# Performance work log

Hardware: AMD Instinct MI355X
Metric: run time of the kernel (lower is better)

## Reference

```python
import jax, jax.numpy as jnp
import numpy as np
import math

SR = 16000
WIN = 320
HOP = 160
NFFT = 512
NMEL = 64
PREEMPH = 0.97
LOG_GUARD = 2.0 ** (-24)
PAD_TO = 16
EPS = 1e-5  # CONSTANT added to std


def _slaney_mel_fbanks(sr=SR, n_fft=NFFT, n_mels=NMEL, fmin=0.0, fmax=8000.0):
    """Replicates torchaudio.functional.melscale_fbanks(norm='slaney', mel_scale='slaney').
    Returns [n_mels, n_freqs] (already transposed like the torch buffer `fb`)."""
    n_freqs = n_fft // 2 + 1
    all_freqs = np.linspace(0.0, sr / 2.0, n_freqs)
    f_sp = 200.0 / 3.0
    min_log_hz = 1000.0
    min_log_mel = min_log_hz / f_sp
    logstep = math.log(6.4) / 27.0

    def hz2mel(f):
        f = np.asarray(f, dtype=np.float64)
        return np.where(f >= min_log_hz,
                        min_log_mel + np.log(np.maximum(f, 1e-10) / min_log_hz) / logstep,
                        f / f_sp)

    def mel2hz(m):
        m = np.asarray(m, dtype=np.float64)
        return np.where(m >= min_log_mel,
                        min_log_hz * np.exp(logstep * (m - min_log_mel)),
                        f_sp * m)

    m_pts = np.linspace(hz2mel(fmin), hz2mel(fmax), n_mels + 2)
    f_pts = mel2hz(m_pts)                       # [n_mels+2]
    f_diff = f_pts[1:] - f_pts[:-1]             # [n_mels+1]
    slopes = f_pts[None, :] - all_freqs[:, None]  # [n_freqs, n_mels+2]
    down = -slopes[:, :-2] / f_diff[:-1]
    up = slopes[:, 2:] / f_diff[1:]
    fb = np.maximum(0.0, np.minimum(down, up))  # [n_freqs, n_mels]
    enorm = 2.0 / (f_pts[2:] - f_pts[:-2])      # slaney area normalization
    fb = fb * enorm[None, :]
    return fb.T.astype(np.float32)              # [n_mels, n_freqs]


def _hann_window_padded(win_length=WIN, n_fft=NFFT):
    # the window symmetrically to n_fft.
    w = np.hanning(win_length).astype(np.float32)
    left = (n_fft - win_length) // 2
    out = np.zeros(n_fft, dtype=np.float32)
    out[left:left + win_length] = w
    return out


def setup_inputs() -> dict:
    key = jax.random.key(0)
    kx, kl = jax.random.split(key)
    B, L = 32, 256000
    x = jax.random.normal(kx, (B, L), dtype=jnp.float32)
    # ragged valid lengths in [L/2, L] (plenty of frames per feature)
    seq_len = jax.random.randint(kl, (B,), L // 2, L + 1, dtype=jnp.int32)
    window = jnp.asarray(_hann_window_padded())       # [NFFT]
    fb = jnp.asarray(_slaney_mel_fbanks())            # [NMEL, NFFT//2+1]
    return {"x": x, "seq_len": seq_len, "window": window, "fb": fb}


def _forward(x, seq_len, window, fb):
    B, L = x.shape
    # get_seq_len: pad_amount = 2*(n_fft//2); floor((L + pad - n_fft)/hop) + 1
    feat_len = (seq_len + NFFT - NFFT) // HOP + 1     # = seq_len // HOP + 1
    # pre-emphasis
    x = jnp.concatenate([x[:, :1], x[:, 1:] - PREEMPH * x[:, :-1]], axis=1)
    # STFT, center=True reflect padding (eval mode: no dither)
    pad = NFFT // 2
    xp = jnp.pad(x, ((0, 0), (pad, pad)), mode='reflect')
    T = L // HOP + 1                                  # 1601 frames
    idx = jnp.arange(T)[:, None] * HOP + jnp.arange(NFFT)[None, :]
    frames = xp[:, idx] * window                      # [B, T, NFFT]
    spec = jnp.fft.rfft(frames, axis=-1)              # [B, T, F]
    # magnitude then mag_power=2 -> power spectrum (guard=0 since use_grads=False)
    pow_spec = spec.real ** 2 + spec.imag ** 2        # [B, T, F]
    mel = jnp.einsum('mf,btf->bmt', fb, pow_spec)     # [B, NMEL, T]
    logmel = jnp.log(mel + LOG_GUARD)
    # per_feature masked normalization (torch.std is unbiased -> /(n-1)), std += 1e-5
    mask = (jnp.arange(T)[None, :] < feat_len[:, None])          # [B, T]
    m = mask[:, None, :].astype(logmel.dtype)                    # [B, 1, T]
    n = feat_len.astype(logmel.dtype)[:, None, None]
    mean = jnp.sum(logmel * m, axis=2, keepdims=True) / n
    var = jnp.sum(((logmel - mean) * m) ** 2, axis=2, keepdims=True) / (n - 1.0)
    std = jnp.sqrt(var) + EPS
    out = (logmel - mean) / std
    # fill padding frames with pad_value=0
    out = jnp.where(m > 0, out, 0.0)
    # pad time dim to a multiple of pad_to=16 with pad_value
    pad_amt = (-T) % PAD_TO
    out = jnp.pad(out, ((0, 0), (0, 0), (0, pad_amt)), constant_values=0.0)
    return out, feat_len


def reference(x, seq_len, window, fb):
    return _forward(x, seq_len, window, fb)
```

## Files before the change

### kernel.cpp

```cpp
#include <hip/hip_runtime.h>
#include <math.h>

#define L_IN 256000
#define T_FR 1601
#define T_PAD 1616
#define NMEL_K 64
#define F_BINS 257
#define HOP_K 160
#define PRE_E 0.97f
#define LOG_GUARD_K 5.9604644775390625e-08f
#define FPB 16
#define CONC 4
#define GROUPS 101
#define SPAN 2912

__device__ __forceinline__ float2 cmulf(float2 a, float2 b) {
  return make_float2(a.x * b.x - a.y * b.y, a.x * b.y + a.y * b.x);
}

__global__ void prep_kernel(const float* __restrict__ fb, float* __restrict__ fbc,
                            int* __restrict__ loAlG) {
  const int m = blockIdx.x;
  const int t = threadIdx.x;
  int first = 512, last = -1;
  for (int c = 0; c < 5; ++c) {
    int f = t + 64 * c;
    if (f < F_BINS) {
      float v = fb[m * F_BINS + f];
      if (v > 0.0f) { first = min(first, f); last = max(last, f); }
    }
  }
  for (int off = 32; off > 0; off >>= 1) {
    first = min(first, __shfl_xor(first, off));
    last = max(last, __shfl_xor(last, off));
  }
  int lo = (first <= last) ? first : 0;
  int lastv = (first <= last) ? last : 0;
  int la = lo & ~3;
  if (t == 0) loAlG[m] = la;
  if (t < 32) {
    int f = la + t;
    float v = (f >= lo && f <= lastv && f < F_BINS) ? fb[m * F_BINS + f] : 0.0f;
    fbc[m * 32 + t] = v;
  }
}

__global__ void __launch_bounds__(256) frame_fft_mel_kernel(
    const float* __restrict__ x, const float* __restrict__ window,
    const float* __restrict__ fbc, const int* __restrict__ loAlG,
    float* __restrict__ out) {
  __shared__ __align__(16) float xs[SPAN];
  __shared__ __align__(16) float pw[CONC][288];
  __shared__ float outm[NMEL_K][FPB + 1];

  const int tid = threadIdx.x;
  const int w = tid >> 6;
  const int lane = tid & 63;
  const int b = blockIdx.x / GROUPS;
  const int g = blockIdx.x - b * GROUPS;
  const int t0 = g * FPB;
  const float* xb = x + (size_t)b * L_IN;
  const int base = t0 * HOP_K - 256;

  for (int n = tid; n < SPAN; n += 256) {
    int i = base + n;
    i = (i < 0) ? -i : i;
    i = (i >= L_IN) ? (2 * L_IN - 2 - i) : i;
    xs[n] = (i == 0) ? xb[0] : fmaf(-PRE_E, xb[i - 1], xb[i]);
  }

  const int sig = __builtin_bitreverse32(lane) >> 26;
  float wr[4], wi[4];
#pragma unroll
  for (int q = 0; q < 4; ++q) {
    float2 wv = *(const float2*)(window + 2 * (lane + 64 * q));
    wr[q] = wv.x; wi[q] = wv.y;
  }
  float2 tw1, tw2, tw3;
  {
    float a = -0.024543692606170259f * (float)lane;
    __sincosf(a, &tw1.y, &tw1.x);
    tw2 = cmulf(tw1, tw1);
    tw3 = cmulf(tw2, tw1);
  }
  float stc[6], sts[6];
#pragma unroll
  for (int i = 0; i < 6; ++i) {
    int H = 32 >> i;
    int p = lane & (H - 1);
    float a = -3.14159265358979323846f * (float)p / (float)H;
    __sincosf(a, &sts[i], &stc[i]);
  }
  float cu[4], su[4];
  {
    float a = -0.049087385212340519f * (float)sig;
    float cb, sb;
    __sincosf(a, &sb, &cb);
    const float C[4] = {1.0f, 0.99992470183914454f, 0.99969881869620425f, 0.99932238458834954f};
    const float S[4] = {0.0f, 0.01227153828571993f, 0.02454122852291229f, 0.03680722294135883f};
#pragma unroll
    for (int r = 0; r < 4; ++r) {
      cu[r] = cb * C[r] + sb * S[r];
      su[r] = sb * C[r] - cb * S[r];
    }
  }
  const int idx0 = __builtin_bitreverse32((64 - sig) & 63) >> 26;
  const int la = loAlG[lane];
  const float4* fr4 = (const float4*)fbc + lane * 8;

  __syncthreads();

  for (int c = 0; c < FPB / CONC; ++c) {
    const int j = c * CONC + w;
    const int off = j * HOP_K;

    float Br[4], Bi[4];
    {
      float zr[4], zi[4];
#pragma unroll
      for (int q = 0; q < 4; ++q) {
        float2 v = *(const float2*)(xs + off + 2 * (lane + 64 * q));
        zr[q] = v.x * wr[q];
        zi[q] = v.y * wi[q];
      }
      float e0r = zr[0] + zr[2], e0i = zi[0] + zi[2];
      float e1r = zr[1] + zr[3], e1i = zi[1] + zi[3];
      float d0r = zr[0] - zr[2], d0i = zi[0] - zi[2];
      float d1r = zr[1] - zr[3], d1i = zi[1] - zi[3];
      Br[0] = e0r + e1r; Bi[0] = e0i + e1i;
      float A2r = e0r - e1r, A2i = e0i - e1i;
      float A1r = d0r + d1i, A1i = d0i - d1r;
      float A3r = d0r - d1i, A3i = d0i + d1r;
      Br[1] = A1r * tw1.x - A1i * tw1.y; Bi[1] = A1r * tw1.y + A1i * tw1.x;
      Br[2] = A2r * tw2.x - A2i * tw2.y; Bi[2] = A2r * tw2.y + A2i * tw2.x;
      Br[3] = A3r * tw3.x - A3i * tw3.y; Bi[3] = A3r * tw3.y + A3i * tw3.x;
    }

#pragma unroll
    for (int i = 0; i < 6; ++i) {
      const int H = 32 >> i;
      const bool hi = (lane & H) != 0;
      const float cc = stc[i], ss = sts[i];
#pragma unroll
      for (int r = 0; r < 4; ++r) {
        float tr = __shfl_xor(Br[r], H);
        float ti = __shfl_xor(Bi[r], H);
        float sr = Br[r] + tr, si = Bi[r] + ti;
        float dr = tr - Br[r], di = ti - Bi[r];
        float pr = dr * cc - di * ss, pi = dr * ss + di * cc;
        Br[r] = hi ? pr : sr;
        Bi[r] = hi ? pi : si;
      }
    }

    {
      float q3r = __shfl_xor(Br[3], 63), q3i = __shfl_xor(Bi[3], 63);
      float q2r = __shfl_xor(Br[2], 63), q2i = __shfl_xor(Bi[2], 63);
      float q1r = __shfl_xor(Br[1], 63), q1i = __shfl_xor(Bi[1], 63);
      float q0r = __shfl(Br[0], idx0), q0i = __shfl(Bi[0], idx0);
      float qr[4] = {q0r, q3r, q2r, q1r};
      float qi_[4] = {q0i, q3i, q2i, q1i};
      float pv[4];
#pragma unroll
      for (int r = 0; r < 4; ++r) {
        float Er = 0.5f * (Br[r] + qr[r]);
        float Ei = 0.5f * (Bi[r] - qi_[r]);
        float Or = 0.5f * (Bi[r] + qi_[r]);
        float Oi = 0.5f * (qr[r] - Br[r]);
        float Xr = Er + cu[r] * Or - su[r] * Oi;
        float Xi = Ei + cu[r] * Oi + su[r] * Or;
        pv[r] = Xr * Xr + Xi * Xi;
      }
      ((float4*)pw[w])[sig] = make_float4(pv[0], pv[1], pv[2], pv[3]);
      if (lane == 0) { float d = Br[0] - Bi[0]; pw[w][256] = d * d; }
      else if (lane < 32) pw[w][256 + lane] = 0.0f;
    }
    __builtin_amdgcn_wave_barrier();

    {
      const float4* pq = (const float4*)pw[w] + (la >> 2);
      float acc = 0.0f;
#pragma unroll
      for (int jj = 0; jj < 8; ++jj) {
        float4 wq = fr4[jj];
        float4 p = pq[jj];
        acc = fmaf(wq.x, p.x, acc);
        acc = fmaf(wq.y, p.y, acc);
        acc = fmaf(wq.z, p.z, acc);
        acc = fmaf(wq.w, p.w, acc);
      }
      outm[lane][j] = __logf(acc + LOG_GUARD_K);
    }
    __builtin_amdgcn_wave_barrier();
  }

  __syncthreads();
#pragma unroll
  for (int p = 0; p < 4; ++p) {
    int row = p * 16 + (tid >> 4);
    int jj = tid & 15;
    int t = t0 + jj;
    if (t < T_FR)
      out[((size_t)b * NMEL_K + row) * T_PAD + t] = outm[row][jj];
  }
}

__global__ void __launch_bounds__(256) norm_kernel(const int* __restrict__ seq_len,
                                                   float* __restrict__ out,
                                                   float* __restrict__ fl_out) {
  const int bm = blockIdx.x;
  const int b = bm >> 6;
  const int m = bm & 63;
  const int tid = threadIdx.x;
  const int fl = seq_len[b] / HOP_K + 1;
  float* row = out + (size_t)bm * T_PAD;
  float vals[7];
  float s = 0.f;
#pragma unroll
  for (int q = 0; q < 7; ++q) {
    int t = q * 256 + tid;
    float v = (t < T_FR) ? row[t] : 0.f;
    vals[q] = v;
    if (t < fl) s += v;
  }
  __shared__ float red[4];
  __shared__ float bc[2];
#pragma unroll
  for (int off = 32; off > 0; off >>= 1) s += __shfl_down(s, off, 64);
  if ((tid & 63) == 0) red[tid >> 6] = s;
  __syncthreads();
  if (tid == 0) bc[0] = (red[0] + red[1] + red[2] + red[3]) / (float)fl;
  __syncthreads();
  const float mean = bc[0];
  float s2 = 0.f;
#pragma unroll
  for (int q = 0; q < 7; ++q) {
    int t = q * 256 + tid;
    if (t < fl) { float d = vals[q] - mean; s2 = fmaf(d, d, s2); }
  }
#pragma unroll
  for (int off = 32; off > 0; off >>= 1) s2 += __shfl_down(s2, off, 64);
  if ((tid & 63) == 0) red[tid >> 6] = s2;
  __syncthreads();
  if (tid == 0) {
    float var = (red[0] + red[1] + red[2] + red[3]) / (float)(fl - 1);
    bc[1] = 1.0f / (sqrtf(var) + 1e-5f);
  }
  __syncthreads();
  const float istd = bc[1];
#pragma unroll
  for (int q = 0; q < 7; ++q) {
    int t = q * 256 + tid;
    if (t < T_PAD) row[t] = (t < fl) ? (vals[q] - mean) * istd : 0.f;
  }
  if (m == 0 && tid == 0) fl_out[b] = (float)fl;
}

extern "C" void kernel_launch(void* const* d_in, const int* in_sizes, int n_in,
                              void* d_out, int out_size, void* d_ws, size_t ws_size,
                              hipStream_t stream) {
  const float* x = (const float*)d_in[0];
  const int* seq_len = (const int*)d_in[1];
  const float* window = (const float*)d_in[2];
  const float* fb = (const float*)d_in[3];
  const int B = in_sizes[1];
  float* out = (float*)d_out;
  float* fl_out = out + (size_t)B * NMEL_K * T_PAD;
  float* fbc = (float*)d_ws;
  int* loAlG = (int*)d_ws + 2048;

  prep_kernel<<<NMEL_K, 64, 0, stream>>>(fb, fbc, loAlG);
  frame_fft_mel_kernel<<<B * GROUPS, 256, 0, stream>>>(x, window, fbc, loAlG, out);
  norm_kernel<<<B * NMEL_K, 256, 0, stream>>>(seq_len, out, fl_out);
}
```

Before: 137.2 us.

## Fuse per-row mean/variance accumulation into FFT kernel via atomics, elementwise normalize

The FFT/mel kernel now accumulates per-(batch, mel) sum and sum-of-squares of the log-mel values inside the valid length and adds them to global buffers with atomics. This replaces the reduction-based norm kernel with a flat elementwise float4 normalize pass. It also adds a vectorized float4 pre-emphasis load path for interior blocks. The aim is to drop the serialized per-row reductions and barriers, at the cost of atomic contention, single-pass variance with weaker numerical stability, and a hardcoded batch size of 32.

Measured after the change: 160.5 us. 17.0% more time.

```diff
diff --git a/kernel.cpp b/kernel.cpp
--- a/kernel.cpp
+++ b/kernel.cpp
@@ -19,9 +19,14 @@
 }
 
 __global__ void prep_kernel(const float* __restrict__ fb, float* __restrict__ fbc,
-                            int* __restrict__ loAlG) {
+                            int* __restrict__ loAl, float* __restrict__ rsum,
+                            float* __restrict__ rsumsq) {
   const int m = blockIdx.x;
   const int t = threadIdx.x;
+  if (t < 32) {
+    rsum[m * 32 + t] = 0.0f;
+    rsumsq[m * 32 + t] = 0.0f;
+  }
   int first = 512, last = -1;
   for (int c = 0; c < 5; ++c) {
     int f = t + 64 * c;
@@ -37,7 +42,7 @@
   int lo = (first <= last) ? first : 0;
   int lastv = (first <= last) ? last : 0;
   int la = lo & ~3;
-  if (t == 0) loAlG[m] = la;
+  if (t == 0) loAl[m] = la;
   if (t < 32) {
     int f = la + t;
     float v = (f >= lo && f <= lastv && f < F_BINS) ? fb[m * F_BINS + f] : 0.0f;
@@ -46,9 +51,10 @@
 }
 
 __global__ void __launch_bounds__(256) frame_fft_mel_kernel(
-    const float* __restrict__ x, const float* __restrict__ window,
-    const float* __restrict__ fbc, const int* __restrict__ loAlG,
-    float* __restrict__ out) {
+    const float* __restrict__ x, const int* __restrict__ seq_len,
+    const float* __restrict__ window, const float* __restrict__ fbc,
+    const int* __restrict__ loAl, float* __restrict__ out,
+    float* __restrict__ rsum, float* __restrict__ rsumsq) {
   __shared__ __align__(16) float xs[SPAN];
   __shared__ __align__(16) float pw[CONC][288];
   __shared__ float outm[NMEL_K][FPB + 1];
@@ -61,12 +67,28 @@
   const int t0 = g * FPB;
   const float* xb = x + (size_t)b * L_IN;
   const int base = t0 * HOP_K - 256;
-
-  for (int n = tid; n < SPAN; n += 256) {
-    int i = base + n;
-    i = (i < 0) ? -i : i;
-    i = (i >= L_IN) ? (2 * L_IN - 2 - i) : i;
-    xs[n] = (i == 0) ? xb[0] : fmaf(-PRE_E, xb[i - 1], xb[i]);
+  const int fl = seq_len[b] / HOP_K + 1;
+
+  if (base >= 0 && base + SPAN <= L_IN) {
+    const float4* xb4 = (const float4*)(xb + base);
+    float4* xs4 = (float4*)xs;
+    for (int s4 = tid; s4 < SPAN / 4; s4 += 256) {
+      float4 cur = xb4[s4];
+      float prev = xb[base + 4 * s4 - 1];
+      float4 o;
+      o.x = fmaf(-PRE_E, prev, cur.x);
+      o.y = fmaf(-PRE_E, cur.x, cur.y);
+      o.z = fmaf(-PRE_E, cur.y, cur.z);
+      o.w = fmaf(-PRE_E, cur.z, cur.w);
+      xs4[s4] = o;
+    }
+  } else {
+    for (int n = tid; n < SPAN; n += 256) {
+      int i = base + n;
+      i = (i < 0) ? -i : i;
+      i = (i >= L_IN) ? (2 * L_IN - 2 - i) : i;
+      xs[n] = (i == 0) ? xb[0] : fmaf(-PRE_E, xb[i - 1], xb[i]);
+    }
   }
 
   const int sig = __builtin_bitreverse32(lane) >> 26;
@@ -105,10 +127,12 @@
     }
   }
   const int idx0 = __builtin_bitreverse32((64 - sig) & 63) >> 26;
-  const int la = loAlG[lane];
+  const int la = loAl[lane];
   const float4* fr4 = (const float4*)fbc + lane * 8;
 
   __syncthreads();
+
+  float sm = 0.0f, ssq = 0.0f;
 
   for (int c = 0; c < FPB / CONC; ++c) {
     const int j = c * CONC + w;
@@ -189,10 +213,15 @@
         acc = fmaf(wq.z, p.z, acc);
         acc = fmaf(wq.w, p.w, acc);
       }
-      outm[lane][j] = __logf(acc + LOG_GUARD_K);
+      float lv = __logf(acc + LOG_GUARD_K);
+      outm[lane][j] = lv;
+      if (t0 + j < fl) { sm += lv; ssq = fmaf(lv, lv, ssq); }
     }
     __builtin_amdgcn_wave_barrier();
   }
+
+  atomicAdd(&rsum[(b << 6) + lane], sm);
+  atomicAdd(&rsumsq[(b << 6) + lane], ssq);
 
   __syncthreads();
 #pragma unroll
@@ -201,59 +230,35 @@
     int jj = tid & 15;
     int t = t0 + jj;
     if (t < T_FR)
-      out[((size_t)b * NMEL_K + row) * T_PAD + t] = outm[row][jj];
-  }
-}
-
-__global__ void __launch_bounds__(256) norm_kernel(const int* __restrict__ seq_len,
-                                                   float* __restrict__ out,
-                                                   float* __restrict__ fl_out) {
-  const int bm = blockIdx.x;
+      out[((size_t)(b << 6) + row) * T_PAD + t] = outm[row][jj];
+  }
+}
+
+__global__ void __launch_bounds__(256) norm_elem_kernel(
+    const int* __restrict__ seq_len, const float* __restrict__ rsum,
+    const float* __restrict__ rsumsq, float* __restrict__ out,
+    float* __restrict__ fl_out) {
+  const int cidx = blockIdx.x * 256 + threadIdx.x;
+  const int bm = cidx / (T_PAD / 4);
+  const int c4 = cidx - bm * (T_PAD / 4);
   const int b = bm >> 6;
-  const int m = bm & 63;
-  const int tid = threadIdx.x;
   const int fl = seq_len[b] / HOP_K + 1;
-  float* row = out + (size_t)bm * T_PAD;
-  float vals[7];
-  float s = 0.f;
-#pragma unroll
-  for (int q = 0; q < 7; ++q) {
-    int t = q * 256 + tid;
-    float v = (t < T_FR) ? row[t] : 0.f;
-    vals[q] = v;
-    if (t < fl) s += v;
-  }
-  __shared__ float red[4];
-  __shared__ float bc[2];
-#pragma unroll
-  for (int off = 32; off > 0; off >>= 1) s += __shfl_down(s, off, 64);
-  if ((tid & 63) == 0) red[tid >> 6] = s;
-  __syncthreads();
-  if (tid == 0) bc[0] = (red[0] + red[1] + red[2] + red[3]) / (float)fl;
-  __syncthreads();
-  const float mean = bc[0];
-  float s2 = 0.f;
-#pragma unroll
-  for (int q = 0; q < 7; ++q) {
-    int t = q * 256 + tid;
-    if (t < fl) { float d = vals[q] - mean; s2 = fmaf(d, d, s2); }
-  }
-#pragma unroll
-  for (int off = 32; off > 0; off >>= 1) s2 += __shfl_down(s2, off, 64);
-  if ((tid & 63) == 0) red[tid >> 6] = s2;
-  __syncthreads();
-  if (tid == 0) {
-    float var = (red[0] + red[1] + red[2] + red[3]) / (float)(fl - 1);
-    bc[1] = 1.0f / (sqrtf(var) + 1e-5f);
-  }
-  __syncthreads();
-  const float istd = bc[1];
-#pragma unroll
-  for (int q = 0; q < 7; ++q) {
-    int t = q * 256 + tid;
-    if (t < T_PAD) row[t] = (t < fl) ? (vals[q] - mean) * istd : 0.f;
-  }
-  if (m == 0 && tid == 0) fl_out[b] = (float)fl;
+  const float n = (float)fl;
+  float s = rsum[bm], ssq = rsumsq[bm];
+  float mean = s / n;
+  float var = (ssq - s * mean) / (n - 1.0f);
+  float istd = 1.0f / (sqrtf(var) + 1e-5f);
+  float4* rowp = (float4*)(out + (size_t)bm * T_PAD);
+  float4 v = rowp[c4];
+  int t = 4 * c4;
+  float4 o;
+  o.x = (t < fl) ? (v.x - mean) * istd : 0.0f;
+  o.y = (t + 1 < fl) ? (v.y - mean) * istd : 0.0f;
+  o.z = (t + 2 < fl) ? (v.z - mean) * istd : 0.0f;
+  o.w = (t + 3 < fl) ? (v.w - mean) * istd : 0.0f;
+  rowp[c4] = o;
+  if (blockIdx.x == 0 && threadIdx.x < 32)
+    fl_out[threadIdx.x] = (float)(seq_len[threadIdx.x] / HOP_K + 1);
 }
 
 extern "C" void kernel_launch(void* const* d_in, const int* in_sizes, int n_in,
@@ -263,13 +268,16 @@
   const int* seq_len = (const int*)d_in[1];
   const float* window = (const float*)d_in[2];
   const float* fb = (const float*)d_in[3];
-  const int B = in_sizes[1];
   float* out = (float*)d_out;
-  float* fl_out = out + (size_t)B * NMEL_K * T_PAD;
+  float* fl_out = out + (size_t)32 * NMEL_K * T_PAD;
   float* fbc = (float*)d_ws;
-  int* loAlG = (int*)d_ws + 2048;
-
-  prep_kernel<<<NMEL_K, 64, 0, stream>>>(fb, fbc, loAlG);
-  frame_fft_mel_kernel<<<B * GROUPS, 256, 0, stream>>>(x, window, fbc, loAlG, out);
-  norm_kernel<<<B * NMEL_K, 256, 0, stream>>>(seq_len, out, fl_out);
-}
+  int* loAl = (int*)((char*)d_ws + 8192);
+  float* rsum = (float*)((char*)d_ws + 8448);
+  float* rsumsq = (float*)((char*)d_ws + 16640);
+
+  prep_kernel<<<NMEL_K, 64, 0, stream>>>(fb, fbc, loAl, rsum, rsumsq);
+  frame_fft_mel_kernel<<<32 * GROUPS, 256, 0, stream>>>(x, seq_len, window, fbc,
+                                                        loAl, out, rsum, rsumsq);
+  norm_elem_kernel<<<(32 * NMEL_K * T_PAD / 4) / 256, 256, 0, stream>>>(
+      seq_len, rsum, rsumsq, out, fl_out);
+}
```
